# Kernel optimization log

Hardware: AMD Instinct MI355X
Metric: run time of the kernel (lower is better)

## Reference

```python
import jax, jax.numpy as jnp
import numpy as np

KS = 32        # kernel_size (chunk size)
STRIDE = 16    # kernel_stride
H = 8          # head_num_k
D = 128        # head_dim
B = 4          # number of sequences
SEQ = 8192     # tokens per sequence (equal-length varlen batch)


def setup_inputs() -> dict:
    key = jax.random.key(0)
    k1, k2, k3, k4, k5 = jax.random.split(key, 5)
    kv = jax.random.normal(k1, (B * SEQ, 2, H, D), dtype=jnp.float32)
    cu_seqlens = jnp.arange(B + 1, dtype=jnp.int32) * SEQ
    # torch Conv1d default init: uniform(-s, s), s = 1/sqrt(in_channels*kernel_size)
    s = 1.0 / np.sqrt(D * KS)
    k_conv_w = jax.random.uniform(k2, (D, D, KS), jnp.float32, -s, s)
    k_conv_b = jax.random.uniform(k3, (D,), jnp.float32, -s, s)
    v_conv_w = jax.random.uniform(k4, (D, D, KS), jnp.float32, -s, s)
    v_conv_b = jax.random.uniform(k5, (D,), jnp.float32, -s, s)
    return {"kv": kv, "cu_seqlens": cu_seqlens,
            "k_conv_w": k_conv_w, "k_conv_b": k_conv_b,
            "v_conv_w": v_conv_w, "v_conv_b": v_conv_b}


def _chunk_indices(cu_seqlens, total_tokens):
    # Equal-length sequences: every strided chunk is valid, so shapes are static.
    batch = cu_seqlens.shape[0] - 1
    seqlen = total_tokens // batch
    nc = (seqlen - KS) // STRIDE + 1  # chunks per sequence
    starts = cu_seqlens[:-1].astype(jnp.int32)          # [B]
    offs = (jnp.arange(nc, dtype=jnp.int32) * STRIDE)   # [nc]
    pos = jnp.arange(KS, dtype=jnp.int32)               # [KS]
    idx = starts[:, None, None] + offs[None, :, None] + pos[None, None, :]  # [B, nc, KS]
    cu_comp = jnp.arange(batch + 1, dtype=jnp.int32) * nc
    return idx.reshape(batch * nc, KS), cu_comp


def reference(kv, cu_seqlens, k_conv_w, k_conv_b, v_conv_w, v_conv_b):
    idx, cu_comp = _chunk_indices(cu_seqlens, kv.shape[0])  # [L, KS]
    filtered = kv[idx.reshape(-1)].reshape(idx.shape[0], KS, 2, H, D)  # [L, KS, 2, H, D]
    k = filtered[:, :, 0]  # [L, KS, H, D]
    v = filtered[:, :, 1]
    # Conv1d with kernel spanning the whole chunk -> single output position:
    # out[l,h,o] = sum_{i,t} x[l,t,h,i] * W[o,i,t] + b[o]
    compress_k = jnp.einsum('lthi,oit->lho', k, k_conv_w) + k_conv_b
    compress_v = jnp.einsum('lthi,oit->lho', v, v_conv_w) + v_conv_b
    return compress_k, compress_v, cu_comp
```

## Files before the change

kernel.cpp:

```cpp
#include <hip/hip_runtime.h>

typedef __attribute__((ext_vector_type(8))) short bf16x8;
typedef __attribute__((ext_vector_type(4))) float f32x4;

#define MFMA16(A, B, C) __builtin_amdgcn_mfma_f32_16x16x32_bf16(A, B, C, 0, 0, 0)

__device__ __forceinline__ unsigned short f2bf(float f) {
  union { float f; unsigned int u; } v; v.f = f;
  return (unsigned short)((v.u + 0x7fffu + ((v.u >> 16) & 1u)) >> 16);
}
#define PK(LO, HI) (((unsigned int)f2bf(LO)) | ((unsigned int)f2bf(HI) << 16))

#define BAR() do {                                              \
    asm volatile("s_waitcnt lgkmcnt(0)" ::: "memory");          \
    __builtin_amdgcn_s_barrier();                               \
    asm volatile("" ::: "memory");                              \
  } while (0)

__global__ __launch_bounds__(256) void prep_kernel(
    const float* __restrict__ kw, const float* __restrict__ vw,
    unsigned short* __restrict__ imgK, unsigned short* __restrict__ imgV,
    int KSd, int dosw,
    const int* __restrict__ cuin, float* __restrict__ outf,
    int cubase, int nb, int strideh) {
  __shared__ float wlds[4096];
  int tid = threadIdx.x, bid = blockIdx.x;
  int sel = bid >> 7, o = bid & 127;
  int nel = 128 * KSd;
  const float* wo = (sel ? vw : kw) + (size_t)o * nel;
  unsigned short* dst = sel ? imgV : imgK;
  for (int i = tid; i < (nel >> 2); i += 256)
    ((float4*)wlds)[i] = ((const float4*)wo)[i];
  __syncthreads();
  int swE = dosw ? ((o & 7) << 3) : 0;
  for (int idx = tid; idx < nel; idx += 256) {
    int s = idx >> 6, c = idx & 63;
    int i = ((s & 1) << 6) + (c ^ swE);
    dst[((size_t)s << 13) + (o << 6) + c] = f2bf(wlds[i * KSd + (s >> 1)]);
  }
  if (bid == 0 && tid <= nb) outf[cubase + tid] = (float)(cuin[tid] / strideh);
}

__global__ __launch_bounds__(512) void gemm_hybrid_kernel(
    const float* __restrict__ kv,
    const float* __restrict__ biasK, const float* __restrict__ biasV,
    const unsigned short* __restrict__ imgK, const unsigned short* __restrict__ imgV,
    float* __restrict__ out,
    int vbase, int nc, int ltot, int tokmax, int seqb, int mtiles) {
  __shared__ __align__(16) unsigned short T[2][66 * 128];
  __shared__ __align__(16) unsigned short Bs[2][8192];
  int tid = threadIdx.x, bid = blockIdx.x;
  int per_sel = 8 * mtiles;
  int sel = (bid >= per_sel) ? 1 : 0;
  int rem = bid - sel * per_sel;
  int h = rem / mtiles, mtile = rem - h * mtiles;
  int m0 = mtile * 64;
  const unsigned short* img = sel ? imgV : imgK;
  const float* bias = sel ? biasV : biasK;
  int outbase = sel ? vbase : 0;
  int lane = tid & 63, wid = tid >> 6;
  int warpM = wid >> 2, warpN = wid & 3;
  int l15 = lane & 15, l4 = lane >> 4;

  int b0 = m0 / nc, c0 = m0 - b0 * nc;
  int btok0 = b0 * seqb + c0 * 16;
  int rb = (b0 + 1) * nc - m0; if (rb > 64) rb = 64;

  int sjl = tid >> 4, sje = tid & 15;
  int soff = sel * 1024 + h * 128 + sje * 8;
  int js0 = sjl, js1 = 32 + sjl, js2 = 64 + sjl;

  int kb0 = l4 * 16;
  int r0 = warpM * 32 + l15, r1 = r0 + 16;
  int j0 = r0 + (r0 >= rb ? 1 : 0);
  int j1 = r1 + (r1 >= rb ? 1 : 0);
  int jb00 = j0 * 256,       jsw00 = (j0 & 7) << 4;
  int jb01 = (j0 + 1) * 256, jsw01 = ((j0 + 1) & 7) << 4;
  int jb10 = j1 * 256,       jsw10 = (j1 & 7) << 4;
  int jb11 = (j1 + 1) * 256, jsw11 = ((j1 + 1) & 7) << 4;

  int o0 = warpN * 32 + l15, o1 = o0 + 16;
  int brb0 = o0 * 128, bsw0 = (o0 & 7) << 4;
  int brb1 = o1 * 128, bsw1 = (o1 & 7) << 4;

  f32x4 zz = {0.f, 0.f, 0.f, 0.f};
  f32x4 acc00 = zz, acc01 = zz, acc10 = zz, acc11 = zz;
  float4 ta0, ta1, ta2, tb0, tb1, tb2;
  uint4 BrA0, BrA1, BrB0, BrB1;

#define STAGE_LOAD(P) do {                                                       \
    int t0_ = btok0 + js0 * 16 + (P); if (t0_ > tokmax) t0_ = tokmax;            \
    const float* a0_ = kv + ((size_t)t0_ << 11) + soff;                          \
    ta0 = *(const float4*)a0_; tb0 = *(const float4*)(a0_ + 4);                  \
    int t1_ = btok0 + js1 * 16 + (P); if (t1_ > tokmax) t1_ = tokmax;            \
    const float* a1_ = kv + ((size_t)t1_ << 11) + soff;                          \
    ta1 = *(const float4*)a1_; tb1 = *(const float4*)(a1_ + 4);                  \
    if (sjl < 2) {                                                               \
      int t2_ = btok0 + js2 * 16 + (P); if (t2_ > tokmax) t2_ = tokmax;          \
      const float* a2_ = kv + ((size_t)t2_ << 11) + soff;                        \
      ta2 = *(const float4*)a2_; tb2 = *(const float4*)(a2_ + 4);                \
    }                                                                            \
  } while (0)

#define T_WRITE(TB) do {                                                         \
    char* tp_ = (char*)(TB);                                                     \
    *(uint4*)(tp_ + js0 * 256 + ((sje * 16) ^ ((js0 & 7) << 4))) =               \
      make_uint4(PK(ta0.x, ta0.y), PK(ta0.z, ta0.w), PK(tb0.x, tb0.y), PK(tb0.z, tb0.w)); \
    *(uint4*)(tp_ + js1 * 256 + ((sje * 16) ^ ((js1 & 7) << 4))) =               \
      make_uint4(PK(ta1.x, ta1.y), PK(ta1.z, ta1.w), PK(tb1.x, tb1.y), PK(tb1.z, tb1.w)); \
    if (sjl < 2)                                                                 \
      *(uint4*)(tp_ + js2 * 256 + ((sje * 16) ^ ((js2 & 7) << 4))) =             \
        make_uint4(PK(ta2.x, ta2.y), PK(ta2.z, ta2.w), PK(tb2.x, tb2.y), PK(tb2.z, tb2.w)); \
  } while (0)

#define B_LOAD(R0, R1, S) do {                                                   \
    const uint4* bsrc_ = (const uint4*)(img + ((size_t)(S) << 13));              \
    R0 = bsrc_[tid];                                                             \
    R1 = bsrc_[512 + tid];                                                       \
  } while (0)

#define B_WRITE(DB, R0, R1) do {                                                 \
    uint4* bdst_ = (uint4*)Bs[DB];                                               \
    bdst_[tid] = R0;                                                             \
    bdst_[512 + tid] = R1;                                                       \
  } while (0)

#define SUBSTEP(HF, JB0, JSW0, JB1, JSW1, BB) do {                               \
    const char* tc_ = (const char*)T[tcur];                                      \
    const char* bc_ = (const char*)Bs[BB];                                       \
    __builtin_amdgcn_s_setprio(1);                                               \
    _Pragma("unroll")                                                            \
    for (int kk = 0; kk < 2; ++kk) {                                             \
      int kcA_ = (HF) * 128 + kk * 64 + kb0;                                     \
      int kcB_ = kk * 64 + kb0;                                                  \
      bf16x8 a0_ = *(const bf16x8*)(tc_ + (JB0) + (kcA_ ^ (JSW0)));              \
      bf16x8 a1_ = *(const bf16x8*)(tc_ + (JB1) + (kcA_ ^ (JSW1)));              \
      bf16x8 b0_ = *(const bf16x8*)(bc_ + brb0 + (kcB_ ^ bsw0));                 \
      bf16x8 b1_ = *(const bf16x8*)(bc_ + brb1 + (kcB_ ^ bsw1));                 \
      acc00 = MFMA16(a0_, b0_, acc00);                                           \
      acc01 = MFMA16(a0_, b1_, acc01);                                           \
      acc10 = MFMA16(a1_, b0_, acc10);                                           \
      acc11 = MFMA16(a1_, b1_, acc11);                                           \
    }                                                                            \
    __builtin_amdgcn_s_setprio(0);                                               \
  } while (0)

  int tcur = 0;
  STAGE_LOAD(0);
  T_WRITE(T[0]);
  B_LOAD(BrA0, BrA1, 0);
  B_WRITE(0, BrA0, BrA1);
  B_LOAD(BrB0, BrB1, 1);
  B_LOAD(BrA0, BrA1, 32);
  BAR();

  for (int p = 0; p < 16; ++p) {
    if (p < 15) STAGE_LOAD(p + 1);
    SUBSTEP(0, jb00, jsw00, jb10, jsw10, 0);
    B_WRITE(1, BrB0, BrB1);
    B_LOAD(BrB0, BrB1, 2 * p + 33);
    BAR();
    SUBSTEP(1, jb00, jsw00, jb10, jsw10, 1);
    B_WRITE(0, BrA0, BrA1);
    if (p < 15) B_LOAD(BrA0, BrA1, 2 * p + 2);
    BAR();
    SUBSTEP(0, jb01, jsw01, jb11, jsw11, 0);
    B_WRITE(1, BrB0, BrB1);
    if (p < 15) B_LOAD(BrB0, BrB1, 2 * p + 3);
    BAR();
    SUBSTEP(1, jb01, jsw01, jb11, jsw11, 1);
    if (p < 15) {
      B_WRITE(0, BrA0, BrA1);
      B_LOAD(BrA0, BrA1, 2 * p + 34);
      T_WRITE(T[tcur ^ 1]);
      BAR();
    }
    tcur ^= 1;
  }

#define STORE_Q(ACC, MI, NI) do {                                                \
    int o_ = warpN * 32 + (NI) * 16 + l15;                                       \
    float bv_ = bias[o_];                                                        \
    int lb_ = m0 + warpM * 32 + (MI) * 16 + l4 * 4;                              \
    _Pragma("unroll")                                                            \
    for (int jj = 0; jj < 4; ++jj) {                                             \
      int ll_ = lb_ + jj;                                                        \
      if (ll_ < ltot)                                                            \
        out[(size_t)outbase + (size_t)ll_ * 1024 + h * 128 + o_] = ACC[jj] + bv_; \
    }                                                                            \
  } while (0)
  STORE_Q(acc00, 0, 0); STORE_Q(acc01, 0, 1);
  STORE_Q(acc10, 1, 0); STORE_Q(acc11, 1, 1);
}

__global__ __launch_bounds__(512) void gemm_kernel(
    const float* __restrict__ kv,
    const float* __restrict__ biasK, const float* __restrict__ biasV,
    const unsigned short* __restrict__ imgK, const unsigned short* __restrict__ imgV,
    const float* __restrict__ kw, const float* __restrict__ vw,
    float* __restrict__ out,
    int selbase, int vbase, int nc, int ltot, int nsteps,
    int tokmax, int seqb, int strideh, int KSd, int mtiles) {
  __shared__ __align__(16) unsigned short As[2][4096];
  __shared__ __align__(16) unsigned short Bsf[2][8192];
  int tid = threadIdx.x, bid = blockIdx.x;
  int per_sel = 8 * mtiles;
  int sel = selbase + (bid >= per_sel);
  int rem = (bid >= per_sel) ? bid - per_sel : bid;
  int h = rem / mtiles, mtile = rem - h * mtiles;
  int m0 = mtile * 64;
  const unsigned short* img = sel ? imgV : imgK;
  const float* bias = sel ? biasV : biasK;
  const float* wsel = sel ? vw : kw;
  int outbase = sel ? vbase : 0;
  int lane = tid & 63, wid = tid >> 6;
  int warpM = wid >> 2, warpN = wid & 3;

  int aj = tid & 7, r = tid >> 3;
  int l = m0 + r; if (l > ltot - 1) l = ltot - 1;
  int b = l / nc, c = l - b * nc;
  int btok = b * seqb + c * strideh;
  const float* abase = kv + sel * 1024 + h * 128 + aj * 4;
  int swr = (r & 7) << 3;
  int awb0 = r * 128 + 2 * ((aj * 4) ^ swr);
  int awb1 = r * 128 + 2 * ((aj * 4 + 32) ^ swr);

  int o_g = tid >> 3, cb_g = (tid & 7) << 3;
  int ib_g = cb_g ^ ((o_g & 7) << 3);
  const float* g0 = wsel + (size_t)o_g * (KSd << 7);
  const float* g1 = g0 + ((size_t)64 * (KSd << 7));

  int kb0 = (lane >> 4) * 16;
  int arb[2], asw[2], brb[2], bsw[2];
#pragma unroll
  for (int mi = 0; mi < 2; ++mi) {
    int rr = warpM * 32 + mi * 16 + (lane & 15);
    arb[mi] = rr * 128; asw[mi] = (rr & 7) << 4;
  }
#pragma unroll
  for (int ni = 0; ni < 2; ++ni) {
    int oo = warpN * 32 + ni * 16 + (lane & 15);
    brb[ni] = oo * 128; bsw[ni] = (oo & 7) << 4;
  }

  f32x4 acc[2][2];
  f32x4 zz = {0.f, 0.f, 0.f, 0.f};
#pragma unroll
  for (int a = 0; a < 2; ++a)
#pragma unroll
    for (int b2 = 0; b2 < 2; ++b2) acc[a][b2] = zz;

  float4 Af0, Af1;
  uint4 Brr[2];

#define LOAD_STEP(S) do {                                                        \
    int tok_ = btok + ((S) >> 1); if (tok_ > tokmax) tok_ = tokmax;              \
    const float* ap_ = abase + ((size_t)tok_ << 11) + (((S) & 1) << 6);          \
    Af0 = *(const float4*)ap_;                                                   \
    Af1 = *(const float4*)(ap_ + 32);                                            \
    if (img) {                                                                   \
      const uint4* bsrc_ = (const uint4*)(img + ((size_t)(S) << 13));            \
      Brr[0] = bsrc_[tid];                                                       \
      Brr[1] = bsrc_[512 + tid];                                                 \
    } else {                                                                     \
      int t_ = (S) >> 1, i0_ = (((S) & 1) << 6) + ib_g;                          \
      unsigned int p0_[4], p1_[4];                                               \
      _Pragma("unroll")                                                          \
      for (int m = 0; m < 4; ++m) {                                              \
        p0_[m] = (unsigned int)f2bf(g0[(i0_ + 2*m) * KSd + t_])                  \
               | ((unsigned int)f2bf(g0[(i0_ + 2*m + 1) * KSd + t_]) << 16);     \
        p1_[m] = (unsigned int)f2bf(g1[(i0_ + 2*m) * KSd + t_])                  \
               | ((unsigned int)f2bf(g1[(i0_ + 2*m + 1) * KSd + t_]) << 16);     \
      }                                                                          \
      Brr[0] = make_uint4(p0_[0], p0_[1], p0_[2], p0_[3]);                       \
      Brr[1] = make_uint4(p1_[0], p1_[1], p1_[2], p1_[3]);                       \
    }                                                                            \
  } while (0)

#define WRITE_STEP(DB) do {                                                      \
    *(uint2*)((char*)As[DB] + awb0) = make_uint2(PK(Af0.x, Af0.y), PK(Af0.z, Af0.w)); \
    *(uint2*)((char*)As[DB] + awb1) = make_uint2(PK(Af1.x, Af1.y), PK(Af1.z, Af1.w)); \
    uint4* bdst_ = (uint4*)Bsf[DB];                                              \
    bdst_[tid] = Brr[0];                                                         \
    bdst_[512 + tid] = Brr[1];                                                   \
  } while (0)

#define COMPUTE_STEP(CB) do {                                                    \
    _Pragma("unroll")                                                            \
    for (int kk = 0; kk < 2; ++kk) {                                             \
      bf16x8 af_[2], bg_[2];                                                     \
      int kc_ = kk * 64 + kb0;                                                   \
      _Pragma("unroll")                                                          \
      for (int mi = 0; mi < 2; ++mi)                                             \
        af_[mi] = *(const bf16x8*)((const char*)As[CB] + arb[mi] + (kc_ ^ asw[mi])); \
      _Pragma("unroll")                                                          \
      for (int ni = 0; ni < 2; ++ni)                                             \
        bg_[ni] = *(const bf16x8*)((const char*)Bsf[CB] + brb[ni] + (kc_ ^ bsw[ni])); \
      _Pragma("unroll")                                                          \
      for (int mi = 0; mi < 2; ++mi)                                             \
      _Pragma("unroll")                                                          \
        for (int ni = 0; ni < 2; ++ni)                                           \
          acc[mi][ni] = MFMA16(af_[mi], bg_[ni], acc[mi][ni]);                   \
    }                                                                            \
  } while (0)

  LOAD_STEP(0);
  WRITE_STEP(0);
  __syncthreads();
  int cur = 0;
  for (int s = 0; s < nsteps; ++s) {
    if (s + 1 < nsteps) LOAD_STEP(s + 1);
    COMPUTE_STEP(cur);
    if (s + 1 < nsteps) WRITE_STEP(cur ^ 1);
    __syncthreads();
    cur ^= 1;
  }

  int l15 = lane & 15, l4 = lane >> 4;
#pragma unroll
  for (int ni = 0; ni < 2; ++ni) {
    int o = warpN * 32 + ni * 16 + l15;
    float bv = bias[o];
#pragma unroll
    for (int mi = 0; mi < 2; ++mi) {
      int lb = m0 + warpM * 32 + mi * 16 + l4 * 4;
      f32x4 v = acc[mi][ni];
#pragma unroll
      for (int jj = 0; jj < 4; ++jj) {
        int ll = lb + jj;
        if (ll < ltot)
          out[(size_t)outbase + (size_t)ll * 1024 + h * 128 + o] = v[jj] + bv;
      }
    }
  }
}

extern "C" void kernel_launch(void* const* d_in, const int* in_sizes, int n_in,
                              void* d_out, int out_size, void* d_ws, size_t ws_size,
                              hipStream_t stream) {
  long kvN = 0; int kvi = 0;
  for (int i = 0; i < n_in; ++i)
    if ((long)in_sizes[i] > kvN) { kvN = in_sizes[i]; kvi = i; }
  const float* kv = (const float*)d_in[kvi];
  const float *w0 = nullptr, *w1 = nullptr, *b0 = nullptr, *b1 = nullptr;
  const int* cuin = nullptr;
  int KSd = 32, nb = 4;
  for (int i = 0; i < n_in; ++i) {
    if (i == kvi) continue;
    int sz = in_sizes[i];
    if (sz == 128) { if (!b0) b0 = (const float*)d_in[i]; else if (!b1) b1 = (const float*)d_in[i]; }
    else if (sz <= 32) { nb = sz - 1; cuin = (const int*)d_in[i]; }
    else if (sz >= 4096) {
      if (!w0) { w0 = (const float*)d_in[i]; KSd = sz / 16384; }
      else if (!w1) w1 = (const float*)d_in[i];
    }
  }
  if (!w0) w0 = (const float*)d_in[2];
  if (!b0) b0 = (const float*)d_in[3];
  if (!w1) w1 = (const float*)d_in[4];
  if (!b1) b1 = (const float*)d_in[5];
  if (!cuin) cuin = (const int*)d_in[1];
  if (nb < 1) nb = 4;

  float* out = (float*)d_out;

  int cubase  = out_size - (nb + 1);
  int vbase   = cubase >> 1;
  int ltot    = cubase >> 11;
  int nc      = ltot / nb;
  int nsteps  = 2 * KSd;
  long tokens = kvN >> 11;
  int seqb    = (int)(tokens / nb);
  int strideh = (nc > 1) ? (seqb - KSd) / (nc - 1) : KSd;
  int tokmax  = (int)tokens - 1;
  int mtiles  = (ltot + 63) >> 6;
  int per_sel = 8 * mtiles;

  size_t imgel = (size_t)nsteps * 8192;
  size_t imgbytes = imgel * 2;
  bool fast = (KSd == 32) && (strideh == 16) && (nc >= 64) &&
              (ws_size >= 2 * imgbytes);
  if (fast) {
    unsigned short* imgK = (unsigned short*)d_ws;
    unsigned short* imgV = imgK + imgel;
    prep_kernel<<<256, 256, 0, stream>>>(w0, w1, imgK, imgV, KSd, 1,
                                         cuin, out, cubase, nb, strideh);
    gemm_hybrid_kernel<<<2 * per_sel, 512, 0, stream>>>(
        kv, b0, b1, imgK, imgV, out, vbase, nc, ltot, tokmax, seqb, mtiles);
  } else if (ws_size >= 2 * imgbytes) {
    unsigned short* imgK = (unsigned short*)d_ws;
    unsigned short* imgV = imgK + imgel;
    prep_kernel<<<256, 256, 0, stream>>>(w0, w1, imgK, imgV, KSd, 1,
                                         cuin, out, cubase, nb, strideh);
    gemm_kernel<<<2 * per_sel, 512, 0, stream>>>(kv, b0, b1, imgK, imgV, w0, w1, out,
        0, vbase, nc, ltot, nsteps, tokmax, seqb, strideh, KSd, mtiles);
  } else {
    prep_kernel<<<256, 256, 0, stream>>>(w0, w1, (unsigned short*)d_ws,
                                         (unsigned short*)d_ws, 0, 1,
                                         cuin, out, cubase, nb, strideh);
    gemm_kernel<<<2 * per_sel, 512, 0, stream>>>(kv, b0, b1,
        (const unsigned short*)nullptr, (const unsigned short*)nullptr, w0, w1, out,
        0, vbase, nc, ltot, nsteps, tokmax, seqb, strideh, KSd, mtiles);
  }
}
```

Baseline: 77.91 us.

## Double M tile to 128 rows per block in fast GEMM path

```diff
diff --git a/kernel.cpp b/kernel.cpp
--- a/kernel.cpp
+++ b/kernel.cpp
@@ -20,7 +20,7 @@
 __global__ __launch_bounds__(256) void prep_kernel(
     const float* __restrict__ kw, const float* __restrict__ vw,
     unsigned short* __restrict__ imgK, unsigned short* __restrict__ imgV,
-    int KSd, int dosw,
+    int KSd,
     const int* __restrict__ cuin, float* __restrict__ outf,
     int cubase, int nb, int strideh) {
   __shared__ float wlds[4096];
@@ -32,7 +32,7 @@
   for (int i = tid; i < (nel >> 2); i += 256)
     ((float4*)wlds)[i] = ((const float4*)wo)[i];
   __syncthreads();
-  int swE = dosw ? ((o & 7) << 3) : 0;
+  int swE = (o & 7) << 3;
   for (int idx = tid; idx < nel; idx += 256) {
     int s = idx >> 6, c = idx & 63;
     int i = ((s & 1) << 6) + (c ^ swE);
@@ -41,76 +41,85 @@
   if (bid == 0 && tid <= nb) outf[cubase + tid] = (float)(cuin[tid] / strideh);
 }
 
-__global__ __launch_bounds__(512) void gemm_hybrid_kernel(
+__global__ __launch_bounds__(512) void gemm_big_kernel(
     const float* __restrict__ kv,
     const float* __restrict__ biasK, const float* __restrict__ biasV,
     const unsigned short* __restrict__ imgK, const unsigned short* __restrict__ imgV,
     float* __restrict__ out,
     int vbase, int nc, int ltot, int tokmax, int seqb, int mtiles) {
-  __shared__ __align__(16) unsigned short T[2][66 * 128];
+  __shared__ __align__(16) unsigned short T[2][16640];
   __shared__ __align__(16) unsigned short Bs[2][8192];
   int tid = threadIdx.x, bid = blockIdx.x;
   int per_sel = 8 * mtiles;
   int sel = (bid >= per_sel) ? 1 : 0;
   int rem = bid - sel * per_sel;
   int h = rem / mtiles, mtile = rem - h * mtiles;
-  int m0 = mtile * 64;
+  int m0 = mtile * 128;
   const unsigned short* img = sel ? imgV : imgK;
   const float* bias = sel ? biasV : biasK;
   int outbase = sel ? vbase : 0;
   int lane = tid & 63, wid = tid >> 6;
-  int warpM = wid >> 2, warpN = wid & 3;
+  int wm = wid >> 2, wn = wid & 3;
   int l15 = lane & 15, l4 = lane >> 4;
 
   int b0 = m0 / nc, c0 = m0 - b0 * nc;
   int btok0 = b0 * seqb + c0 * 16;
-  int rb = (b0 + 1) * nc - m0; if (rb > 64) rb = 64;
+  int rb = nc - c0;
 
   int sjl = tid >> 4, sje = tid & 15;
   int soff = sel * 1024 + h * 128 + sje * 8;
-  int js0 = sjl, js1 = 32 + sjl, js2 = 64 + sjl;
 
   int kb0 = l4 * 16;
-  int r0 = warpM * 32 + l15, r1 = r0 + 16;
-  int j0 = r0 + (r0 >= rb ? 1 : 0);
-  int j1 = r1 + (r1 >= rb ? 1 : 0);
-  int jb00 = j0 * 256,       jsw00 = (j0 & 7) << 4;
-  int jb01 = (j0 + 1) * 256, jsw01 = ((j0 + 1) & 7) << 4;
-  int jb10 = j1 * 256,       jsw10 = (j1 & 7) << 4;
-  int jb11 = (j1 + 1) * 256, jsw11 = ((j1 + 1) & 7) << 4;
-
-  int o0 = warpN * 32 + l15, o1 = o0 + 16;
+  int jbL[4], jswL[4], jbH[4], jswH[4];
+#pragma unroll
+  for (int mi = 0; mi < 4; ++mi) {
+    int r = wm * 64 + mi * 16 + l15;
+    int j = r + (r >= rb ? 1 : 0);
+    jbL[mi] = j * 256;       jswL[mi] = (j & 7) << 4;
+    jbH[mi] = (j + 1) * 256; jswH[mi] = ((j + 1) & 7) << 4;
+  }
+
+  int o0 = wn * 32 + l15, o1 = o0 + 16;
   int brb0 = o0 * 128, bsw0 = (o0 & 7) << 4;
   int brb1 = o1 * 128, bsw1 = (o1 & 7) << 4;
 
   f32x4 zz = {0.f, 0.f, 0.f, 0.f};
-  f32x4 acc00 = zz, acc01 = zz, acc10 = zz, acc11 = zz;
-  float4 ta0, ta1, ta2, tb0, tb1, tb2;
+  f32x4 acc[4][2];
+#pragma unroll
+  for (int mi = 0; mi < 4; ++mi) { acc[mi][0] = zz; acc[mi][1] = zz; }
+
+  float4 ta[5], tb[5];
   uint4 BrA0, BrA1, BrB0, BrB1;
 
 #define STAGE_LOAD(P) do {                                                       \
-    int t0_ = btok0 + js0 * 16 + (P); if (t0_ > tokmax) t0_ = tokmax;            \
-    const float* a0_ = kv + ((size_t)t0_ << 11) + soff;                          \
-    ta0 = *(const float4*)a0_; tb0 = *(const float4*)(a0_ + 4);                  \
-    int t1_ = btok0 + js1 * 16 + (P); if (t1_ > tokmax) t1_ = tokmax;            \
-    const float* a1_ = kv + ((size_t)t1_ << 11) + soff;                          \
-    ta1 = *(const float4*)a1_; tb1 = *(const float4*)(a1_ + 4);                  \
+    _Pragma("unroll")                                                            \
+    for (int q_ = 0; q_ < 4; ++q_) {                                             \
+      int t_ = btok0 + (q_ * 32 + sjl) * 16 + (P); if (t_ > tokmax) t_ = tokmax; \
+      const float* a_ = kv + ((size_t)t_ << 11) + soff;                          \
+      ta[q_] = *(const float4*)a_; tb[q_] = *(const float4*)(a_ + 4);            \
+    }                                                                            \
     if (sjl < 2) {                                                               \
-      int t2_ = btok0 + js2 * 16 + (P); if (t2_ > tokmax) t2_ = tokmax;          \
-      const float* a2_ = kv + ((size_t)t2_ << 11) + soff;                        \
-      ta2 = *(const float4*)a2_; tb2 = *(const float4*)(a2_ + 4);                \
+      int t_ = btok0 + (128 + sjl) * 16 + (P); if (t_ > tokmax) t_ = tokmax;     \
+      const float* a_ = kv + ((size_t)t_ << 11) + soff;                          \
+      ta[4] = *(const float4*)a_; tb[4] = *(const float4*)(a_ + 4);              \
     }                                                                            \
   } while (0)
 
 #define T_WRITE(TB) do {                                                         \
     char* tp_ = (char*)(TB);                                                     \
-    *(uint4*)(tp_ + js0 * 256 + ((sje * 16) ^ ((js0 & 7) << 4))) =               \
-      make_uint4(PK(ta0.x, ta0.y), PK(ta0.z, ta0.w), PK(tb0.x, tb0.y), PK(tb0.z, tb0.w)); \
-    *(uint4*)(tp_ + js1 * 256 + ((sje * 16) ^ ((js1 & 7) << 4))) =               \
-      make_uint4(PK(ta1.x, ta1.y), PK(ta1.z, ta1.w), PK(tb1.x, tb1.y), PK(tb1.z, tb1.w)); \
-    if (sjl < 2)                                                                 \
-      *(uint4*)(tp_ + js2 * 256 + ((sje * 16) ^ ((js2 & 7) << 4))) =             \
-        make_uint4(PK(ta2.x, ta2.y), PK(ta2.z, ta2.w), PK(tb2.x, tb2.y), PK(tb2.z, tb2.w)); \
+    _Pragma("unroll")                                                            \
+    for (int q_ = 0; q_ < 4; ++q_) {                                             \
+      int js_ = q_ * 32 + sjl;                                                   \
+      *(uint4*)(tp_ + js_ * 256 + ((sje * 16) ^ ((js_ & 7) << 4))) =             \
+        make_uint4(PK(ta[q_].x, ta[q_].y), PK(ta[q_].z, ta[q_].w),               \
+                   PK(tb[q_].x, tb[q_].y), PK(tb[q_].z, tb[q_].w));              \
+    }                                                                            \
+    if (sjl < 2) {                                                               \
+      int js_ = 128 + sjl;                                                       \
+      *(uint4*)(tp_ + js_ * 256 + ((sje * 16) ^ ((js_ & 7) << 4))) =             \
+        make_uint4(PK(ta[4].x, ta[4].y), PK(ta[4].z, ta[4].w),                   \
+                   PK(tb[4].x, tb[4].y), PK(tb[4].z, tb[4].w));                  \
+    }                                                                            \
   } while (0)
 
 #define B_LOAD(R0, R1, S) do {                                                   \
@@ -125,7 +134,7 @@
     bdst_[512 + tid] = R1;                                                       \
   } while (0)
 
-#define SUBSTEP(HF, JB0, JSW0, JB1, JSW1, BB) do {                               \
+#define SUBSTEP(HF, JB, JSW, BB) do {                                            \
     const char* tc_ = (const char*)T[tcur];                                      \
     const char* bc_ = (const char*)Bs[BB];                                       \
     __builtin_amdgcn_s_setprio(1);                                               \
@@ -133,14 +142,14 @@
     for (int kk = 0; kk < 2; ++kk) {                                             \
       int kcA_ = (HF) * 128 + kk * 64 + kb0;                                     \
       int kcB_ = kk * 64 + kb0;                                                  \
-      bf16x8 a0_ = *(const bf16x8*)(tc_ + (JB0) + (kcA_ ^ (JSW0)));              \
-      bf16x8 a1_ = *(const bf16x8*)(tc_ + (JB1) + (kcA_ ^ (JSW1)));              \
       bf16x8 b0_ = *(const bf16x8*)(bc_ + brb0 + (kcB_ ^ bsw0));                 \
       bf16x8 b1_ = *(const bf16x8*)(bc_ + brb1 + (kcB_ ^ bsw1));                 \
-      acc00 = MFMA16(a0_, b0_, acc00);                                           \
-      acc01 = MFMA16(a0_, b1_, acc01);                                           \
-      acc10 = MFMA16(a1_, b0_, acc10);                                           \
-      acc11 = MFMA16(a1_, b1_, acc11);                                           \
+      _Pragma("unroll")                                                          \
+      for (int mi = 0; mi < 4; ++mi) {                                           \
+        bf16x8 a_ = *(const bf16x8*)(tc_ + JB[mi] + (kcA_ ^ JSW[mi]));           \
+        acc[mi][0] = MFMA16(a_, b0_, acc[mi][0]);                                \
+        acc[mi][1] = MFMA16(a_, b1_, acc[mi][1]);                                \
+      }                                                                          \
     }                                                                            \
     __builtin_amdgcn_s_setprio(0);                                               \
   } while (0)
@@ -156,19 +165,19 @@
 
   for (int p = 0; p < 16; ++p) {
     if (p < 15) STAGE_LOAD(p + 1);
-    SUBSTEP(0, jb00, jsw00, jb10, jsw10, 0);
+    SUBSTEP(0, jbL, jswL, 0);
     B_WRITE(1, BrB0, BrB1);
     B_LOAD(BrB0, BrB1, 2 * p + 33);
     BAR();
-    SUBSTEP(1, jb00, jsw00, jb10, jsw10, 1);
+    SUBSTEP(1, jbL, jswL, 1);
     B_WRITE(0, BrA0, BrA1);
     if (p < 15) B_LOAD(BrA0, BrA1, 2 * p + 2);
     BAR();
-    SUBSTEP(0, jb01, jsw01, jb11, jsw11, 0);
+    SUBSTEP(0, jbH, jswH, 0);
     B_WRITE(1, BrB0, BrB1);
     if (p < 15) B_LOAD(BrB0, BrB1, 2 * p + 3);
     BAR();
-    SUBSTEP(1, jb01, jsw01, jb11, jsw11, 1);
+    SUBSTEP(1, jbH, jswH, 1);
     if (p < 15) {
       B_WRITE(0, BrA0, BrA1);
       B_LOAD(BrA0, BrA1, 2 * p + 34);
@@ -178,19 +187,22 @@
     tcur ^= 1;
   }
 
-#define STORE_Q(ACC, MI, NI) do {                                                \
-    int o_ = warpN * 32 + (NI) * 16 + l15;                                       \
-    float bv_ = bias[o_];                                                        \
-    int lb_ = m0 + warpM * 32 + (MI) * 16 + l4 * 4;                              \
-    _Pragma("unroll")                                                            \
-    for (int jj = 0; jj < 4; ++jj) {                                             \
-      int ll_ = lb_ + jj;                                                        \
-      if (ll_ < ltot)                                                            \
-        out[(size_t)outbase + (size_t)ll_ * 1024 + h * 128 + o_] = ACC[jj] + bv_; \
-    }                                                                            \
-  } while (0)
-  STORE_Q(acc00, 0, 0); STORE_Q(acc01, 0, 1);
-  STORE_Q(acc10, 1, 0); STORE_Q(acc11, 1, 1);
+#pragma unroll
+  for (int ni = 0; ni < 2; ++ni) {
+    int o_ = wn * 32 + ni * 16 + l15;
+    float bv_ = bias[o_];
+#pragma unroll
+    for (int mi = 0; mi < 4; ++mi) {
+      int lb_ = m0 + wm * 64 + mi * 16 + l4 * 4;
+      f32x4 v_ = acc[mi][ni];
+#pragma unroll
+      for (int jj = 0; jj < 4; ++jj) {
+        int ll_ = lb_ + jj;
+        if (ll_ < ltot)
+          out[(size_t)outbase + (size_t)ll_ * 1024 + h * 128 + o_] = v_[jj] + bv_;
+      }
+    }
+  }
 }
 
 __global__ __launch_bounds__(512) void gemm_kernel(
@@ -374,29 +386,30 @@
   int strideh = (nc > 1) ? (seqb - KSd) / (nc - 1) : KSd;
   int tokmax  = (int)tokens - 1;
   int mtiles  = (ltot + 63) >> 6;
+  int mt128   = (ltot + 127) >> 7;
   int per_sel = 8 * mtiles;
 
   size_t imgel = (size_t)nsteps * 8192;
   size_t imgbytes = imgel * 2;
-  bool fast = (KSd == 32) && (strideh == 16) && (nc >= 64) &&
+  bool fast = (KSd == 32) && (strideh == 16) && (nc >= 128) &&
               (ws_size >= 2 * imgbytes);
   if (fast) {
     unsigned short* imgK = (unsigned short*)d_ws;
     unsigned short* imgV = imgK + imgel;
-    prep_kernel<<<256, 256, 0, stream>>>(w0, w1, imgK, imgV, KSd, 1,
+    prep_kernel<<<256, 256, 0, stream>>>(w0, w1, imgK, imgV, KSd,
                                          cuin, out, cubase, nb, strideh);
-    gemm_hybrid_kernel<<<2 * per_sel, 512, 0, stream>>>(
-        kv, b0, b1, imgK, imgV, out, vbase, nc, ltot, tokmax, seqb, mtiles);
+    gemm_big_kernel<<<2 * 8 * mt128, 512, 0, stream>>>(
+        kv, b0, b1, imgK, imgV, out, vbase, nc, ltot, tokmax, seqb, mt128);
   } else if (ws_size >= 2 * imgbytes) {
     unsigned short* imgK = (unsigned short*)d_ws;
     unsigned short* imgV = imgK + imgel;
-    prep_kernel<<<256, 256, 0, stream>>>(w0, w1, imgK, imgV, KSd, 1,
+    prep_kernel<<<256, 256, 0, stream>>>(w0, w1, imgK, imgV, KSd,
                                          cuin, out, cubase, nb, strideh);
     gemm_kernel<<<2 * per_sel, 512, 0, stream>>>(kv, b0, b1, imgK, imgV, w0, w1, out,
         0, vbase, nc, ltot, nsteps, tokmax, seqb, strideh, KSd, mtiles);
   } else {
     prep_kernel<<<256, 256, 0, stream>>>(w0, w1, (unsigned short*)d_ws,
-                                         (unsigned short*)d_ws, 0, 1,
+                                         (unsigned short*)d_ws, 0,
                                          cuin, out, cubase, nb, strideh);
     gemm_kernel<<<2 * per_sel, 512, 0, stream>>>(kv, b0, b1,
         (const unsigned short*)nullptr, (const unsigned short*)nullptr, w0, w1, out,
```

Measured after the change: 77.44 us. No clear change (-0.6%).
